# Optimization experiments

Hardware: AMD Instinct MI355X
Metric: run time of the kernel (lower is better)

Reference implementation:

```python
import jax, jax.numpy as jnp
import numpy as np

N_NODES = 100000
N_EDGES = 1600000
DIMS = [128, 128, 128, 64]


def setup_inputs() -> dict:
    key = jax.random.key(0)
    ks = jax.random.split(key, 12)
    inp = {
        "features": jax.random.normal(ks[0], (N_NODES, DIMS[0]), dtype=jnp.float32),
        "src": jax.random.randint(ks[1], (N_EDGES,), 0, N_NODES, dtype=jnp.int64),
        "dst": jax.random.randint(ks[2], (N_EDGES,), 0, N_NODES, dtype=jnp.int64),
        "edge_weight": jax.random.uniform(ks[3], (N_EDGES,), dtype=jnp.float32),
    }
    # GraphConv weights (xavier-like scale) and biases per layer
    for i in range(3):
        fin, fout = DIMS[i], DIMS[i + 1]
        scale = (2.0 / (fin + fout)) ** 0.5
        inp[f"W{i}"] = jax.random.normal(ks[4 + i], (fin, fout), dtype=jnp.float32) * scale
        inp[f"b{i}"] = jnp.zeros((fout,), dtype=jnp.float32)
    return inp


def _graph_conv(h, W, b, src, dst, ew, out_norm, in_norm):
    # DGL GraphConv, norm='both', with per-edge weight (u_mul_e message).
    fin, fout = W.shape
    h = h * out_norm[:, None]
    if fin > fout:  # mult W first to reduce message width
        h = h @ W
    msg = h[src] * ew[:, None]                       # [E, d] irregular gather
    agg = jax.ops.segment_sum(msg, dst, num_segments=N_NODES)
    agg = agg * in_norm[:, None]
    if fin <= fout:
        agg = agg @ W
    return agg + b


def reference(features, src, dst, edge_weight, W0, b0, W1, b1, W2, b2):
    ones = jnp.ones((N_EDGES,), dtype=features.dtype)
    out_deg = jax.ops.segment_sum(ones, src, num_segments=N_NODES)
    in_deg = jax.ops.segment_sum(ones, dst, num_segments=N_NODES)
    out_norm = jnp.clip(out_deg, 1.0, None) ** -0.5
    in_norm = jnp.clip(in_deg, 1.0, None) ** -0.5
    h = features
    Ws = [(W0, b0), (W1, b1), (W2, b2)]
    for i, (W, b) in enumerate(Ws):
        h = _graph_conv(h, W, b, src, dst, edge_weight, out_norm, in_norm)
        if i < len(Ws) - 1:
            h = jax.nn.relu(h)
    return h
```

## Files before the change

kernel.cpp:

```cpp
#include <hip/hip_runtime.h>
#include <cstddef>
#include <cstdint>

typedef float f4 __attribute__((ext_vector_type(4)));
typedef unsigned long long u64;
typedef unsigned short u16;
typedef unsigned char u8;
typedef unsigned short u16x8 __attribute__((ext_vector_type(8)));
typedef short short8 __attribute__((ext_vector_type(8)));

__device__ __forceinline__ u64 ldnt8(const void* p) {
    return __builtin_nontemporal_load((const u64*)(p));
}
__device__ __forceinline__ u16 bfrn(float f) {
    unsigned u = __float_as_uint(f);
    return (u16)((u + 0x7FFFu + ((u >> 16) & 1u)) >> 16);
}
__device__ __forceinline__ float bl(unsigned w) { return __uint_as_float(w << 16); }
__device__ __forceinline__ float bh(unsigned w) { return __uint_as_float(w & 0xFFFF0000u); }


#define EPB 4096

__global__ void __launch_bounds__(256)
k_p1(const int* __restrict__ src, const int* __restrict__ dst,
     int* __restrict__ bh_s, int* __restrict__ bh_d, int NB, int E) {
    __shared__ int hs[512], hd[512];
    const int t = threadIdx.x, b = blockIdx.x;
    for (int i = t; i < 512; i += 256) { hs[i] = 0; hd[i] = 0; }
    __syncthreads();
    const int e0 = b * EPB;
    #pragma unroll
    for (int j = 0; j < 4; ++j) {
        const int e = e0 + j * 1024 + t * 4;
        if (e + 4 <= E) {
            const int4 d = *(const int4*)&dst[e];
            const int4 s = *(const int4*)&src[e];
            atomicAdd(&hd[d.x >> 8], 1);
            atomicAdd(&hd[d.y >> 8], 1);
            atomicAdd(&hd[d.z >> 8], 1);
            atomicAdd(&hd[d.w >> 8], 1);
            atomicAdd(&hs[s.x >> 8], 1);
            atomicAdd(&hs[s.y >> 8], 1);
            atomicAdd(&hs[s.z >> 8], 1);
            atomicAdd(&hs[s.w >> 8], 1);
        } else {
            for (int k = e; k < E && k < e + 4; ++k) {
                atomicAdd(&hd[dst[k] >> 8], 1);
                atomicAdd(&hs[src[k] >> 8], 1);
            }
        }
    }
    __syncthreads();
    for (int i = t; i < NB; i += 256) {
        bh_d[b * NB + i] = hd[i];
        bh_s[b * NB + i] = hs[i];
    }
}

__global__ void __launch_bounds__(512)
k_p2(int* __restrict__ bh_d, int* __restrict__ bh_s,
     int* __restrict__ cb_d, int* __restrict__ cb_s, int NB, int B1) {
    __shared__ int s[512];
    const int B = blockIdx.x, i = threadIdx.x;
    int* bh = blockIdx.y ? bh_s : bh_d;
    int* cb = blockIdx.y ? cb_s : cb_d;
    const int v = (i < B1) ? bh[i * NB + B] : 0;
    s[i] = v;
    __syncthreads();
    for (int off = 1; off < 512; off <<= 1) {
        const int x = (i >= off) ? s[i - off] : 0;
        __syncthreads();
        s[i] += x;
        __syncthreads();
    }
    if (i < B1) bh[i * NB + B] = s[i] - v;
    if (i == 511) cb[B] = s[511];
}

__global__ void __launch_bounds__(512)
k_p2b(const int* __restrict__ cb_d, const int* __restrict__ cb_s,
      int* __restrict__ bktb_d, int* __restrict__ bktb_s,
      int* __restrict__ row, int NB, int N, int E) {
    __shared__ int s[512];
    const int t = threadIdx.x;
    int v = (t < NB) ? cb_d[t] : 0;
    s[t] = v;
    __syncthreads();
    for (int off = 1; off < 512; off <<= 1) {
        const int x = (t >= off) ? s[t - off] : 0;
        __syncthreads();
        s[t] += x;
        __syncthreads();
    }
    if (t < NB) bktb_d[t] = s[t] - v;
    __syncthreads();
    v = (t < NB) ? cb_s[t] : 0;
    s[t] = v;
    __syncthreads();
    for (int off = 1; off < 512; off <<= 1) {
        const int x = (t >= off) ? s[t - off] : 0;
        __syncthreads();
        s[t] += x;
        __syncthreads();
    }
    if (t < NB) bktb_s[t] = s[t] - v;
    if (t == 0) row[N] = E;
}

__global__ void __launch_bounds__(256)
k_p3(const int* __restrict__ src, const int* __restrict__ dst,
     const float* __restrict__ ew,
     const int* __restrict__ bh_s, const int* __restrict__ bh_d,
     const int* __restrict__ bktb_s, const int* __restrict__ bktb_d,
     int2* __restrict__ tsw, u8* __restrict__ tsrc, int NB, int E) {
    __shared__ int hs[512], hd[512], base_s[512], base_d[512];
    const int t = threadIdx.x, b = blockIdx.x;
    for (int i = t; i < 512; i += 256) {
        hs[i] = 0; hd[i] = 0;
        if (i < NB) {
            base_d[i] = bktb_d[i] + bh_d[b * NB + i];
            base_s[i] = bktb_s[i] + bh_s[b * NB + i];
        }
    }
    __syncthreads();
    const int e0 = b * EPB;
    #pragma unroll
    for (int j = 0; j < 4; ++j) {
        const int e = e0 + j * 1024 + t * 4;
        if (e + 4 <= E) {
            const int4 d = *(const int4*)&dst[e];
            const int4 s = *(const int4*)&src[e];
            const f4   w = *(const f4*)&ew[e];
            const int dd[4] = {d.x, d.y, d.z, d.w};
            const int ss[4] = {s.x, s.y, s.z, s.w};
            const float ww[4] = {w.x, w.y, w.z, w.w};
            #pragma unroll
            for (int k = 0; k < 4; ++k) {
                const int Bd = dd[k] >> 8;
                const int rd = atomicAdd(&hd[Bd], 1);
                tsw[base_d[Bd] + rd] = make_int2(ss[k] | ((dd[k] & 255) << 24),
                                                 __float_as_int(ww[k]));
                const int Bs = ss[k] >> 8;
                const int rs = atomicAdd(&hs[Bs], 1);
                tsrc[base_s[Bs] + rs] = (u8)(ss[k] & 255);
            }
        } else {
            for (int k = e; k < E && k < e + 4; ++k) {
                const int dv = dst[k], sv = src[k];
                const int Bd = dv >> 8;
                const int rd = atomicAdd(&hd[Bd], 1);
                tsw[base_d[Bd] + rd] = make_int2(sv | ((dv & 255) << 24),
                                                 __float_as_int(ew[k]));
                const int Bs = sv >> 8;
                const int rs = atomicAdd(&hs[Bs], 1);
                tsrc[base_s[Bs] + rs] = (u8)(sv & 255);
            }
        }
    }
}

__global__ void __launch_bounds__(256)
k_p4s(const u8* __restrict__ tsrc, const int* __restrict__ bktb_s,
      const int* __restrict__ cb_s, float* __restrict__ onorm, int NB, int N) {
    __shared__ int cnt[256];
    const int B = blockIdx.x, t = threadIdx.x;
    cnt[t] = 0;
    __syncthreads();
    const int base = bktb_s[B], cb = cb_s[B];
    for (int i = t; i < cb; i += 256) atomicAdd(&cnt[tsrc[base + i]], 1);
    __syncthreads();
    const int n = (B << 8) + t;
    if (n < N) {
        const int c = cnt[t];
        onorm[n] = rsqrtf((float)(c < 1 ? 1 : c));
    }
}

__global__ void __launch_bounds__(256)
k_p4d(const int2* __restrict__ tsw,
      const int* __restrict__ bktb_d, const int* __restrict__ cb_d,
      const float* __restrict__ onorm, int* __restrict__ row,
      float* __restrict__ inorm, int2* __restrict__ csr, int NB, int N) {
    __shared__ int cnt[256], cnt2[256], lrow[256], sc[256];
    const int B = blockIdx.x, t = threadIdx.x;
    cnt[t] = 0; cnt2[t] = 0;
    __syncthreads();
    const int base = bktb_d[B], cb = cb_d[B];
    for (int i = t; i < cb; i += 256)
        atomicAdd(&cnt[((unsigned)tsw[base + i].x) >> 24], 1);
    __syncthreads();
    const int v = cnt[t];
    sc[t] = v;
    __syncthreads();
    for (int off = 1; off < 256; off <<= 1) {
        const int x = (t >= off) ? sc[t - off] : 0;
        __syncthreads();
        sc[t] += x;
        __syncthreads();
    }
    const int excl = sc[t] - v;
    lrow[t] = excl;
    const int n = (B << 8) + t;
    if (n < N) {
        row[n] = base + excl;
        inorm[n] = rsqrtf((float)(v < 1 ? 1 : v));
    }
    __syncthreads();
    for (int i = t; i < cb; i += 256) {
        const int2 sw = tsw[base + i];
        const int d = ((unsigned)sw.x) >> 24;
        const int s = sw.x & 0xFFFFFF;
        const int r = atomicAdd(&cnt2[d], 1);
        const float coef = __int_as_float(sw.y) * onorm[s];
        csr[base + lrow[d] + r] = make_int2(s, __float_as_int(coef));
    }
}

__global__ void __launch_bounds__(256)
k_cvt(const float* __restrict__ in, u16* __restrict__ out, int n8) {
    const int i = blockIdx.x * blockDim.x + threadIdx.x;
    if (i < n8) {
        const f4 v0 = *(const f4*)(in + (size_t)i * 8);
        const f4 v1 = *(const f4*)(in + (size_t)i * 8 + 4);
        u16x8 r = {bfrn(v0.x), bfrn(v0.y), bfrn(v0.z), bfrn(v0.w),
                   bfrn(v1.x), bfrn(v1.y), bfrn(v1.z), bfrn(v1.w)};
        *(u16x8*)(out + (size_t)i * 8) = r;
    }
}

__global__ void __launch_bounds__(256)
k_wcvt3(const float* __restrict__ W0, const float* __restrict__ W1,
        const float* __restrict__ W2, u16* __restrict__ Wt0,
        u16* __restrict__ Wt1, u16* __restrict__ Wt2) {
    const int i = blockIdx.x * 256 + threadIdx.x;
    if (i < 16384) {
        const int k = i >> 7, c = i & 127;
        Wt0[c * 128 + k] = bfrn(W0[i]);
    } else if (i < 32768) {
        const int j = i - 16384, k = j >> 7, c = j & 127;
        Wt1[c * 128 + k] = bfrn(W1[j]);
    } else if (i < 40960) {
        const int j = i - 32768, k = j >> 6, c = j & 63;
        Wt2[c * 128 + k] = bfrn(W2[j]);
    }
}

__global__ void __launch_bounds__(256)
k_agg128b(const u16* __restrict__ h, const int* __restrict__ row,
          const int2* __restrict__ csr, const float* __restrict__ inorm,
          u16* __restrict__ out, int N) {
    const int node = (int)((blockIdx.x * blockDim.x + threadIdx.x) >> 6);
    if (node >= N) return;
    const int lane = threadIdx.x & 63;
    const int q = lane >> 4;
    const int col = (lane & 15) * 8;
    int p = row[node];
    const int e = row[node + 1];
    float a0 = 0, a1 = 0, a2 = 0, a3 = 0, a4 = 0, a5 = 0, a6 = 0, a7 = 0;
    for (; p + 16 <= e; p += 16) {
        const u64 c0 = ldnt8(&csr[p + q]);
        const u64 c1 = ldnt8(&csr[p + 4 + q]);
        const u64 c2 = ldnt8(&csr[p + 8 + q]);
        const u64 c3 = ldnt8(&csr[p + 12 + q]);
        const uint4 w0 = *(const uint4*)(h + (size_t)(int)c0 * 128 + col);
        const uint4 w1 = *(const uint4*)(h + (size_t)(int)c1 * 128 + col);
        const uint4 w2 = *(const uint4*)(h + (size_t)(int)c2 * 128 + col);
        const uint4 w3 = *(const uint4*)(h + (size_t)(int)c3 * 128 + col);
        const float f0 = __int_as_float((int)(c0 >> 32));
        const float f1 = __int_as_float((int)(c1 >> 32));
        const float f2 = __int_as_float((int)(c2 >> 32));
        const float f3 = __int_as_float((int)(c3 >> 32));
        a0 = fmaf(f0, bl(w0.x), a0); a1 = fmaf(f0, bh(w0.x), a1);
        a2 = fmaf(f0, bl(w0.y), a2); a3 = fmaf(f0, bh(w0.y), a3);
        a4 = fmaf(f0, bl(w0.z), a4); a5 = fmaf(f0, bh(w0.z), a5);
        a6 = fmaf(f0, bl(w0.w), a6); a7 = fmaf(f0, bh(w0.w), a7);
        a0 = fmaf(f1, bl(w1.x), a0); a1 = fmaf(f1, bh(w1.x), a1);
        a2 = fmaf(f1, bl(w1.y), a2); a3 = fmaf(f1, bh(w1.y), a3);
        a4 = fmaf(f1, bl(w1.z), a4); a5 = fmaf(f1, bh(w1.z), a5);
        a6 = fmaf(f1, bl(w1.w), a6); a7 = fmaf(f1, bh(w1.w), a7);
        a0 = fmaf(f2, bl(w2.x), a0); a1 = fmaf(f2, bh(w2.x), a1);
        a2 = fmaf(f2, bl(w2.y), a2); a3 = fmaf(f2, bh(w2.y), a3);
        a4 = fmaf(f2, bl(w2.z), a4); a5 = fmaf(f2, bh(w2.z), a5);
        a6 = fmaf(f2, bl(w2.w), a6); a7 = fmaf(f2, bh(w2.w), a7);
        a0 = fmaf(f3, bl(w3.x), a0); a1 = fmaf(f3, bh(w3.x), a1);
        a2 = fmaf(f3, bl(w3.y), a2); a3 = fmaf(f3, bh(w3.y), a3);
        a4 = fmaf(f3, bl(w3.z), a4); a5 = fmaf(f3, bh(w3.z), a5);
        a6 = fmaf(f3, bl(w3.w), a6); a7 = fmaf(f3, bh(w3.w), a7);
    }
    for (; p + 8 <= e; p += 8) {
        const u64 c0 = ldnt8(&csr[p + q]);
        const u64 c1 = ldnt8(&csr[p + 4 + q]);
        const uint4 w0 = *(const uint4*)(h + (size_t)(int)c0 * 128 + col);
        const uint4 w1 = *(const uint4*)(h + (size_t)(int)c1 * 128 + col);
        const float f0 = __int_as_float((int)(c0 >> 32));
        const float f1 = __int_as_float((int)(c1 >> 32));
        a0 = fmaf(f0, bl(w0.x), a0); a1 = fmaf(f0, bh(w0.x), a1);
        a2 = fmaf(f0, bl(w0.y), a2); a3 = fmaf(f0, bh(w0.y), a3);
        a4 = fmaf(f0, bl(w0.z), a4); a5 = fmaf(f0, bh(w0.z), a5);
        a6 = fmaf(f0, bl(w0.w), a6); a7 = fmaf(f0, bh(w0.w), a7);
        a0 = fmaf(f1, bl(w1.x), a0); a1 = fmaf(f1, bh(w1.x), a1);
        a2 = fmaf(f1, bl(w1.y), a2); a3 = fmaf(f1, bh(w1.y), a3);
        a4 = fmaf(f1, bl(w1.z), a4); a5 = fmaf(f1, bh(w1.z), a5);
        a6 = fmaf(f1, bl(w1.w), a6); a7 = fmaf(f1, bh(w1.w), a7);
    }
    {
        const int i0 = p + q, i1 = p + 4 + q;
        if (i0 < e) {
            const u64 c = ldnt8(&csr[i0]);
            const uint4 w = *(const uint4*)(h + (size_t)(int)c * 128 + col);
            const float f = __int_as_float((int)(c >> 32));
            a0 = fmaf(f, bl(w.x), a0); a1 = fmaf(f, bh(w.x), a1);
            a2 = fmaf(f, bl(w.y), a2); a3 = fmaf(f, bh(w.y), a3);
            a4 = fmaf(f, bl(w.z), a4); a5 = fmaf(f, bh(w.z), a5);
            a6 = fmaf(f, bl(w.w), a6); a7 = fmaf(f, bh(w.w), a7);
        }
        if (i1 < e) {
            const u64 c = ldnt8(&csr[i1]);
            const uint4 w = *(const uint4*)(h + (size_t)(int)c * 128 + col);
            const float f = __int_as_float((int)(c >> 32));
            a0 = fmaf(f, bl(w.x), a0); a1 = fmaf(f, bh(w.x), a1);
            a2 = fmaf(f, bl(w.y), a2); a3 = fmaf(f, bh(w.y), a3);
            a4 = fmaf(f, bl(w.z), a4); a5 = fmaf(f, bh(w.z), a5);
            a6 = fmaf(f, bl(w.w), a6); a7 = fmaf(f, bh(w.w), a7);
        }
    }
    a0 += __shfl_xor(a0, 16); a1 += __shfl_xor(a1, 16);
    a2 += __shfl_xor(a2, 16); a3 += __shfl_xor(a3, 16);
    a4 += __shfl_xor(a4, 16); a5 += __shfl_xor(a5, 16);
    a6 += __shfl_xor(a6, 16); a7 += __shfl_xor(a7, 16);
    a0 += __shfl_xor(a0, 32); a1 += __shfl_xor(a1, 32);
    a2 += __shfl_xor(a2, 32); a3 += __shfl_xor(a3, 32);
    a4 += __shfl_xor(a4, 32); a5 += __shfl_xor(a5, 32);
    a6 += __shfl_xor(a6, 32); a7 += __shfl_xor(a7, 32);
    if (lane < 16) {
        const float nn = inorm[node];
        u16x8 r = {bfrn(a0 * nn), bfrn(a1 * nn), bfrn(a2 * nn), bfrn(a3 * nn),
                   bfrn(a4 * nn), bfrn(a5 * nn), bfrn(a6 * nn), bfrn(a7 * nn)};
        *(u16x8*)(out + (size_t)node * 128 + col) = r;
    }
}

__global__ void __launch_bounds__(256)
k_agg64b(const u16* __restrict__ h, const int* __restrict__ row,
         const int2* __restrict__ csr, const float* __restrict__ inorm,
         const float* __restrict__ bias, float* __restrict__ out, int N) {
    const int node = (int)((blockIdx.x * blockDim.x + threadIdx.x) >> 6);
    if (node >= N) return;
    const int lane = threadIdx.x & 63;
    const int oc = lane >> 3;
    const int col = (lane & 7) * 8;
    int p = row[node];
    const int e = row[node + 1];
    float a0 = 0, a1 = 0, a2 = 0, a3 = 0, a4 = 0, a5 = 0, a6 = 0, a7 = 0;
    for (; p + 16 <= e; p += 16) {
        const u64 c0 = ldnt8(&csr[p + oc]);
        const u64 c1 = ldnt8(&csr[p + 8 + oc]);
        const uint4 w0 = *(const uint4*)(h + (size_t)(int)c0 * 64 + col);
        const uint4 w1 = *(const uint4*)(h + (size_t)(int)c1 * 64 + col);
        const float f0 = __int_as_float((int)(c0 >> 32));
        const float f1 = __int_as_float((int)(c1 >> 32));
        a0 = fmaf(f0, bl(w0.x), a0); a1 = fmaf(f0, bh(w0.x), a1);
        a2 = fmaf(f0, bl(w0.y), a2); a3 = fmaf(f0, bh(w0.y), a3);
        a4 = fmaf(f0, bl(w0.z), a4); a5 = fmaf(f0, bh(w0.z), a5);
        a6 = fmaf(f0, bl(w0.w), a6); a7 = fmaf(f0, bh(w0.w), a7);
        a0 = fmaf(f1, bl(w1.x), a0); a1 = fmaf(f1, bh(w1.x), a1);
        a2 = fmaf(f1, bl(w1.y), a2); a3 = fmaf(f1, bh(w1.y), a3);
        a4 = fmaf(f1, bl(w1.z), a4); a5 = fmaf(f1, bh(w1.z), a5);
        a6 = fmaf(f1, bl(w1.w), a6); a7 = fmaf(f1, bh(w1.w), a7);
    }
    {
        const int i0 = p + oc, i1 = p + 8 + oc;
        if (i0 < e) {
            const u64 c = ldnt8(&csr[i0]);
            const uint4 w = *(const uint4*)(h + (size_t)(int)c * 64 + col);
            const float f = __int_as_float((int)(c >> 32));
            a0 = fmaf(f, bl(w.x), a0); a1 = fmaf(f, bh(w.x), a1);
            a2 = fmaf(f, bl(w.y), a2); a3 = fmaf(f, bh(w.y), a3);
            a4 = fmaf(f, bl(w.z), a4); a5 = fmaf(f, bh(w.z), a5);
            a6 = fmaf(f, bl(w.w), a6); a7 = fmaf(f, bh(w.w), a7);
        }
        if (i1 < e) {
            const u64 c = ldnt8(&csr[i1]);
            const uint4 w = *(const uint4*)(h + (size_t)(int)c * 64 + col);
            const float f = __int_as_float((int)(c >> 32));
            a0 = fmaf(f, bl(w.x), a0); a1 = fmaf(f, bh(w.x), a1);
            a2 = fmaf(f, bl(w.y), a2); a3 = fmaf(f, bh(w.y), a3);
            a4 = fmaf(f, bl(w.z), a4); a5 = fmaf(f, bh(w.z), a5);
            a6 = fmaf(f, bl(w.w), a6); a7 = fmaf(f, bh(w.w), a7);
        }
    }
    a0 += __shfl_xor(a0, 8);  a1 += __shfl_xor(a1, 8);
    a2 += __shfl_xor(a2, 8);  a3 += __shfl_xor(a3, 8);
    a4 += __shfl_xor(a4, 8);  a5 += __shfl_xor(a5, 8);
    a6 += __shfl_xor(a6, 8);  a7 += __shfl_xor(a7, 8);
    a0 += __shfl_xor(a0, 16); a1 += __shfl_xor(a1, 16);
    a2 += __shfl_xor(a2, 16); a3 += __shfl_xor(a3, 16);
    a4 += __shfl_xor(a4, 16); a5 += __shfl_xor(a5, 16);
    a6 += __shfl_xor(a6, 16); a7 += __shfl_xor(a7, 16);
    a0 += __shfl_xor(a0, 32); a1 += __shfl_xor(a1, 32);
    a2 += __shfl_xor(a2, 32); a3 += __shfl_xor(a3, 32);
    a4 += __shfl_xor(a4, 32); a5 += __shfl_xor(a5, 32);
    a6 += __shfl_xor(a6, 32); a7 += __shfl_xor(a7, 32);
    if (lane < 8) {
        const float nn = inorm[node];
        const f4 b0 = *(const f4*)(bias + col);
        const f4 b1 = *(const f4*)(bias + col + 4);
        f4 r0 = {a0 * nn + b0.x, a1 * nn + b0.y, a2 * nn + b0.z, a3 * nn + b0.w};
        f4 r1 = {a4 * nn + b1.x, a5 * nn + b1.y, a6 * nn + b1.z, a7 * nn + b1.w};
        *(f4*)(out + (size_t)node * 64 + col) = r0;
        *(f4*)(out + (size_t)node * 64 + col + 4) = r1;
    }
}

template <int COLS, bool RELU, bool BIAS>
__global__ void __launch_bounds__(256)
k_mgemm(const u16* __restrict__ A, const u16* __restrict__ Wt,
        const float* __restrict__ bias, u16* __restrict__ C, int N) {
    __shared__ u16 Wl[COLS][136];
    const int t = threadIdx.x;
    const int lane = t & 63;
    const int wave = t >> 6;
    #pragma unroll
    for (int i = 0; i < COLS / 16; ++i) {
        const int elem = (i * 256 + t) * 8;
        const int r = elem >> 7, c0 = elem & 127;
        *(short8*)&Wl[r][c0] = *(const short8*)(Wt + elem);
    }
    const int row0 = blockIdx.x * 64 + wave * 16;
    const int arow = min(row0 + (lane & 15), N - 1);
    const int koff = (lane >> 4) * 8;
    short8 a[4];
    #pragma unroll
    for (int kk = 0; kk < 4; ++kk)
        a[kk] = *(const short8*)(A + (size_t)arow * 128 + kk * 32 + koff);
    __syncthreads();

    f4 acc[COLS / 16];
    #pragma unroll
    for (int ct = 0; ct < COLS / 16; ++ct) acc[ct] = (f4){0.f, 0.f, 0.f, 0.f};

    #pragma unroll
    for (int ct = 0; ct < COLS / 16; ++ct) {
        #pragma unroll
        for (int kk = 0; kk < 4; ++kk) {
            const short8 b = *(const short8*)&Wl[ct * 16 + (lane & 15)][kk * 32 + koff];
            acc[ct] = __builtin_amdgcn_mfma_f32_16x16x32_bf16(a[kk], b, acc[ct], 0, 0, 0);
        }
    }

    #pragma unroll
    for (int ct = 0; ct < COLS / 16; ++ct) {
        const int c = ct * 16 + (lane & 15);
        const float bb = BIAS ? bias[c] : 0.f;
        #pragma unroll
        for (int r = 0; r < 4; ++r) {
            const int gr = row0 + (lane >> 4) * 4 + r;
            if (gr < N) {
                float v = acc[ct][r] + bb;
                if (RELU) v = v > 0.f ? v : 0.f;
                C[(size_t)gr * COLS + c] = bfrn(v);
            }
        }
    }
}

extern "C" void kernel_launch(void* const* d_in, const int* in_sizes, int n_in,
                              void* d_out, int out_size, void* d_ws, size_t ws_size,
                              hipStream_t stream) {
    const float* feat = (const float*)d_in[0];
    const int*   src  = (const int*)d_in[1];
    const int*   dst  = (const int*)d_in[2];
    const float* ew   = (const float*)d_in[3];
    const float* W0   = (const float*)d_in[4];
    const float* b0   = (const float*)d_in[5];
    const float* W1   = (const float*)d_in[6];
    const float* b1   = (const float*)d_in[7];
    const float* W2   = (const float*)d_in[8];
    const float* b2   = (const float*)d_in[9];
    float* out = (float*)d_out;

    const int N = in_sizes[0] / 128;
    const int E = in_sizes[1];
    const int NB = (N + 255) / 256;
    const int B1 = (E + EPB - 1) / EPB;

    uint8_t* wp = (uint8_t*)d_ws;
    auto alloc = [&](size_t bytes) {
        uint8_t* r = wp;
        wp += (bytes + 511) & ~(size_t)511;
        return r;
    };
    u16*   featb = (u16*)alloc((size_t)N * 128 * 2);
    u16*   Xb    = (u16*)alloc((size_t)N * 128 * 2);
    u16*   Tb    = (u16*)alloc((size_t)N * 128 * 2);
    u8*    scr   = (u8*)alloc((size_t)E * 10 + 65536);
    int2*  csr   = (int2*)alloc((size_t)E * 8);
    int*   row   = (int*)alloc((size_t)(N + 1) * 4);
    float* onorm = (float*)alloc((size_t)N * 4);
    float* inorm = (float*)alloc((size_t)N * 4);
    u16*   Wt0   = (u16*)alloc(128 * 128 * 2);
    u16*   Wt1   = (u16*)alloc(128 * 128 * 2);
    u16*   Wt2   = (u16*)alloc(128 * 64 * 2);

    uint8_t* xp = (uint8_t*)Xb;
    auto xalloc = [&](size_t bytes) {
        uint8_t* r = xp;
        xp += (bytes + 511) & ~(size_t)511;
        return r;
    };
    int* bh_d   = (int*)xalloc((size_t)B1 * NB * 4);
    int* bh_s   = (int*)xalloc((size_t)B1 * NB * 4);
    int* cb_d   = (int*)xalloc((size_t)NB * 4);
    int* cb_s   = (int*)xalloc((size_t)NB * 4);
    int* bktb_d = (int*)xalloc((size_t)NB * 4);
    int* bktb_s = (int*)xalloc((size_t)NB * 4);

    uint8_t* yp = scr;
    auto yalloc = [&](size_t bytes) {
        uint8_t* r = yp;
        yp += (bytes + 511) & ~(size_t)511;
        return r;
    };
    int2* tsw  = (int2*)yalloc((size_t)E * 8);
    u8*   tsrc = (u8*)yalloc((size_t)E);
    u16*  Gb   = (u16*)scr;

    k_cvt<<<(N * 128 / 8 + 255) / 256, 256, 0, stream>>>(feat, featb, N * 128 / 8);
    k_wcvt3<<<160, 256, 0, stream>>>(W0, W1, W2, Wt0, Wt1, Wt2);
    k_p1<<<B1, 256, 0, stream>>>(src, dst, bh_s, bh_d, NB, E);
    k_p2<<<dim3(NB, 2), 512, 0, stream>>>(bh_d, bh_s, cb_d, cb_s, NB, B1);
    k_p2b<<<1, 512, 0, stream>>>(cb_d, cb_s, bktb_d, bktb_s, row, NB, N, E);
    k_p3<<<B1, 256, 0, stream>>>(src, dst, ew, bh_s, bh_d, bktb_s, bktb_d,
                                 tsw, tsrc, NB, E);
    k_p4s<<<NB, 256, 0, stream>>>(tsrc, bktb_s, cb_s, onorm, NB, N);
    k_p4d<<<NB, 256, 0, stream>>>(tsw, bktb_d, cb_d, onorm, row, inorm, csr, NB, N);

    const int ab = (N + 3) / 4;
    const int gb = (N + 63) / 64;

    k_agg128b<<<ab, 256, 0, stream>>>(featb, row, csr, inorm, Tb, N);
    k_mgemm<128, true, true><<<gb, 256, 0, stream>>>(Tb, Wt0, b0, Xb, N);
    k_agg128b<<<ab, 256, 0, stream>>>(Xb, row, csr, inorm, Tb, N);
    k_mgemm<128, true, true><<<gb, 256, 0, stream>>>(Tb, Wt1, b1, featb, N);
    k_mgemm<64, false, false><<<gb, 256, 0, stream>>>(featb, Wt2, nullptr, Gb, N);
    k_agg64b<<<ab, 256, 0, stream>>>(Gb, row, csr, inorm, b2, out, N);
}
```

Before: 313.4 us.

## Merge histogram and conversion kernels, tile column scan in k_p2

```diff
diff --git a/kernel.cpp b/kernel.cpp
--- a/kernel.cpp
+++ b/kernel.cpp
@@ -23,59 +23,113 @@
 #define EPB 4096
 
 __global__ void __launch_bounds__(256)
-k_p1(const int* __restrict__ src, const int* __restrict__ dst,
-     int* __restrict__ bh_s, int* __restrict__ bh_d, int NB, int E) {
-    __shared__ int hs[512], hd[512];
-    const int t = threadIdx.x, b = blockIdx.x;
-    for (int i = t; i < 512; i += 256) { hs[i] = 0; hd[i] = 0; }
-    __syncthreads();
-    const int e0 = b * EPB;
-    #pragma unroll
-    for (int j = 0; j < 4; ++j) {
-        const int e = e0 + j * 1024 + t * 4;
-        if (e + 4 <= E) {
-            const int4 d = *(const int4*)&dst[e];
-            const int4 s = *(const int4*)&src[e];
-            atomicAdd(&hd[d.x >> 8], 1);
-            atomicAdd(&hd[d.y >> 8], 1);
-            atomicAdd(&hd[d.z >> 8], 1);
-            atomicAdd(&hd[d.w >> 8], 1);
-            atomicAdd(&hs[s.x >> 8], 1);
-            atomicAdd(&hs[s.y >> 8], 1);
-            atomicAdd(&hs[s.z >> 8], 1);
-            atomicAdd(&hs[s.w >> 8], 1);
-        } else {
-            for (int k = e; k < E && k < e + 4; ++k) {
-                atomicAdd(&hd[dst[k] >> 8], 1);
-                atomicAdd(&hs[src[k] >> 8], 1);
+k_prep0(const int* __restrict__ src, const int* __restrict__ dst,
+        int* __restrict__ bh_s, int* __restrict__ bh_d,
+        const float* __restrict__ feat, u16* __restrict__ featb, int n8,
+        const float* __restrict__ W0, const float* __restrict__ W1,
+        const float* __restrict__ W2, u16* __restrict__ Wt0,
+        u16* __restrict__ Wt1, u16* __restrict__ Wt2,
+        int NB, int B1, int E) {
+    const int bid = blockIdx.x, t = threadIdx.x;
+    if (bid < B1) {
+        __shared__ int hs[512], hd[512];
+        for (int i = t; i < 512; i += 256) { hs[i] = 0; hd[i] = 0; }
+        __syncthreads();
+        const int e0 = bid * EPB;
+        #pragma unroll
+        for (int j = 0; j < 4; ++j) {
+            const int e = e0 + j * 1024 + t * 4;
+            if (e + 4 <= E) {
+                const int4 d = *(const int4*)&dst[e];
+                const int4 s = *(const int4*)&src[e];
+                atomicAdd(&hd[d.x >> 8], 1);
+                atomicAdd(&hd[d.y >> 8], 1);
+                atomicAdd(&hd[d.z >> 8], 1);
+                atomicAdd(&hd[d.w >> 8], 1);
+                atomicAdd(&hs[s.x >> 8], 1);
+                atomicAdd(&hs[s.y >> 8], 1);
+                atomicAdd(&hs[s.z >> 8], 1);
+                atomicAdd(&hs[s.w >> 8], 1);
+            } else {
+                for (int k = e; k < E && k < e + 4; ++k) {
+                    atomicAdd(&hd[dst[k] >> 8], 1);
+                    atomicAdd(&hs[src[k] >> 8], 1);
+                }
             }
         }
-    }
-    __syncthreads();
-    for (int i = t; i < NB; i += 256) {
-        bh_d[b * NB + i] = hd[i];
-        bh_s[b * NB + i] = hs[i];
+        __syncthreads();
+        for (int i = t; i < NB; i += 256) {
+            bh_d[bid * NB + i] = hd[i];
+            bh_s[bid * NB + i] = hs[i];
+        }
+    } else if (bid < B1 + (n8 + 255) / 256) {
+        const int i = (bid - B1) * 256 + t;
+        if (i < n8) {
+            const f4 v0 = *(const f4*)(feat + (size_t)i * 8);
+            const f4 v1 = *(const f4*)(feat + (size_t)i * 8 + 4);
+            u16x8 r = {bfrn(v0.x), bfrn(v0.y), bfrn(v0.z), bfrn(v0.w),
+                       bfrn(v1.x), bfrn(v1.y), bfrn(v1.z), bfrn(v1.w)};
+            *(u16x8*)(featb + (size_t)i * 8) = r;
+        }
+    } else {
+        const int i = (bid - B1 - (n8 + 255) / 256) * 256 + t;
+        if (i < 16384) {
+            const int k = i >> 7, c = i & 127;
+            Wt0[c * 128 + k] = bfrn(W0[i]);
+        } else if (i < 32768) {
+            const int j = i - 16384, k = j >> 7, c = j & 127;
+            Wt1[c * 128 + k] = bfrn(W1[j]);
+        } else if (i < 40960) {
+            const int j = i - 32768, k = j >> 6, c = j & 63;
+            Wt2[c * 128 + k] = bfrn(W2[j]);
+        }
     }
 }
 
 __global__ void __launch_bounds__(512)
 k_p2(int* __restrict__ bh_d, int* __restrict__ bh_s,
      int* __restrict__ cb_d, int* __restrict__ cb_s, int NB, int B1) {
-    __shared__ int s[512];
-    const int B = blockIdx.x, i = threadIdx.x;
+    __shared__ int tile[512][17];
+    __shared__ int tot[16];
+    const int t = threadIdx.x, lane = t & 63, wave = t >> 6;
     int* bh = blockIdx.y ? bh_s : bh_d;
     int* cb = blockIdx.y ? cb_s : cb_d;
-    const int v = (i < B1) ? bh[i * NB + B] : 0;
-    s[i] = v;
-    __syncthreads();
-    for (int off = 1; off < 512; off <<= 1) {
-        const int x = (i >= off) ? s[i - off] : 0;
-        __syncthreads();
-        s[i] += x;
-        __syncthreads();
-    }
-    if (i < B1) bh[i * NB + B] = s[i] - v;
-    if (i == 511) cb[B] = s[511];
+    const int B0 = blockIdx.x * 16;
+    #pragma unroll
+    for (int j = 0; j < 16; ++j) {
+        const int idx = j * 512 + t;
+        const int row = idx >> 4, col = idx & 15;
+        int v = 0;
+        if (row < B1 && B0 + col < NB) v = bh[row * NB + B0 + col];
+        tile[row][col] = v;
+    }
+    __syncthreads();
+    #pragma unroll
+    for (int cc = 0; cc < 2; ++cc) {
+        const int col = wave * 2 + cc;
+        int carry = 0;
+        #pragma unroll
+        for (int ch = 0; ch < 8; ++ch) {
+            const int v = tile[ch * 64 + lane][col];
+            int s = v;
+            #pragma unroll
+            for (int d = 1; d < 64; d <<= 1) {
+                const int u = __shfl_up(s, d);
+                if (lane >= d) s += u;
+            }
+            tile[ch * 64 + lane][col] = s - v + carry;
+            carry += __shfl(s, 63);
+        }
+        if (lane == 0) tot[col] = carry;
+    }
+    __syncthreads();
+    #pragma unroll
+    for (int j = 0; j < 16; ++j) {
+        const int idx = j * 512 + t;
+        const int row = idx >> 4, col = idx & 15;
+        if (row < B1 && B0 + col < NB) bh[row * NB + B0 + col] = tile[row][col];
+    }
+    if (t < 16 && B0 + t < NB) cb[B0 + t] = tot[t];
 }
 
 __global__ void __launch_bounds__(512)
@@ -214,35 +268,6 @@
         const int r = atomicAdd(&cnt2[d], 1);
         const float coef = __int_as_float(sw.y) * onorm[s];
         csr[base + lrow[d] + r] = make_int2(s, __float_as_int(coef));
-    }
-}
-
-__global__ void __launch_bounds__(256)
-k_cvt(const float* __restrict__ in, u16* __restrict__ out, int n8) {
-    const int i = blockIdx.x * blockDim.x + threadIdx.x;
-    if (i < n8) {
-        const f4 v0 = *(const f4*)(in + (size_t)i * 8);
-        const f4 v1 = *(const f4*)(in + (size_t)i * 8 + 4);
-        u16x8 r = {bfrn(v0.x), bfrn(v0.y), bfrn(v0.z), bfrn(v0.w),
-                   bfrn(v1.x), bfrn(v1.y), bfrn(v1.z), bfrn(v1.w)};
-        *(u16x8*)(out + (size_t)i * 8) = r;
-    }
-}
-
-__global__ void __launch_bounds__(256)
-k_wcvt3(const float* __restrict__ W0, const float* __restrict__ W1,
-        const float* __restrict__ W2, u16* __restrict__ Wt0,
-        u16* __restrict__ Wt1, u16* __restrict__ Wt2) {
-    const int i = blockIdx.x * 256 + threadIdx.x;
-    if (i < 16384) {
-        const int k = i >> 7, c = i & 127;
-        Wt0[c * 128 + k] = bfrn(W0[i]);
-    } else if (i < 32768) {
-        const int j = i - 16384, k = j >> 7, c = j & 127;
-        Wt1[c * 128 + k] = bfrn(W1[j]);
-    } else if (i < 40960) {
-        const int j = i - 32768, k = j >> 6, c = j & 63;
-        Wt2[c * 128 + k] = bfrn(W2[j]);
     }
 }
 
@@ -484,6 +509,7 @@
     const int E = in_sizes[1];
     const int NB = (N + 255) / 256;
     const int B1 = (E + EPB - 1) / EPB;
+    const int n8 = N * 16;
 
     uint8_t* wp = (uint8_t*)d_ws;
     auto alloc = [&](size_t bytes) {
@@ -526,10 +552,11 @@
     u8*   tsrc = (u8*)yalloc((size_t)E);
     u16*  Gb   = (u16*)scr;
 
-    k_cvt<<<(N * 128 / 8 + 255) / 256, 256, 0, stream>>>(feat, featb, N * 128 / 8);
-    k_wcvt3<<<160, 256, 0, stream>>>(W0, W1, W2, Wt0, Wt1, Wt2);
-    k_p1<<<B1, 256, 0, stream>>>(src, dst, bh_s, bh_d, NB, E);
-    k_p2<<<dim3(NB, 2), 512, 0, stream>>>(bh_d, bh_s, cb_d, cb_s, NB, B1);
+    const int nbcvt = (n8 + 255) / 256;
+    k_prep0<<<B1 + nbcvt + 160, 256, 0, stream>>>(
+        src, dst, bh_s, bh_d, feat, featb, n8,
+        W0, W1, W2, Wt0, Wt1, Wt2, NB, B1, E);
+    k_p2<<<dim3((NB + 15) / 16, 2), 512, 0, stream>>>(bh_d, bh_s, cb_d, cb_s, NB, B1);
     k_p2b<<<1, 512, 0, stream>>>(cb_d, cb_s, bktb_d, bktb_s, row, NB, N, E);
     k_p3<<<B1, 256, 0, stream>>>(src, dst, ew, bh_s, bh_d, bktb_s, bktb_d,
                                  tsw, tsrc, NB, E);
```

Result: no change. 311.3 us (-0.7%).
